# Kernel optimization log

Measured on AMD Instinct MI355X. Metric: run time of the kernel, lower is better.

The kernel has to match this reference:

```python
import jax, jax.numpy as jnp
import numpy as np

NUM_EXPERTS = 4
MLP_RATIO = 4


def setup_inputs() -> dict:
    key = jax.random.key(0)
    k1, k2, k3, k4, k5, k6 = jax.random.split(key, 6)
    B, N, D = 4, 4096, 1024
    OUT = 1024
    H = D * MLP_RATIO
    x = jax.random.normal(k1, (B, N, D), dtype=jnp.float32)
    expert_mask = jax.random.randint(k2, (B, N), 0, NUM_EXPERTS, dtype=jnp.int64)
    w1 = jax.random.normal(k3, (H, D), dtype=jnp.float32) * 0.02
    b1 = jax.random.normal(k4, (H,), dtype=jnp.float32) * 0.02
    w2 = jax.random.normal(k5, (OUT, H), dtype=jnp.float32) * 0.02
    b2 = jax.random.normal(k6, (OUT,), dtype=jnp.float32) * 0.02
    return {"x": x, "expert_mask": expert_mask, "w1": w1, "b1": b1, "w2": w2, "b2": b2}


def reference(x, expert_mask, w1, b1, w2, b2):
    # x: [B, N, D]; expert_mask: [B, N] in [0, NUM_EXPERTS)
    D = x.shape[-1]
    OUT = w2.shape[0]
    E = NUM_EXPERTS
    y = jnp.zeros(x.shape[:-1] + (OUT,), dtype=x.dtype)
    for e in range(E):
        shift = E - 1 - e  # expert E-1 uses full width
        d_in = D >> shift
        d_hid = d_in * MLP_RATIO
        d_out = OUT >> shift
        # nested slice of shared weights
        h = jax.nn.gelu(
            jnp.einsum('bnd,hd->bnh', x[..., :d_in], w1[:d_hid, :d_in]) + b1[:d_hid],
            approximate=False,
        )
        ye = jnp.einsum('bnh,oh->bno', h, w2[:d_out, :d_hid]) + b2[:d_out]
        ye = jnp.pad(ye, ((0, 0), (0, 0), (0, OUT - d_out)))  # zero-fill unused dims
        y = y + jnp.where((expert_mask == e)[..., None], ye, jnp.zeros((), dtype=x.dtype))
    return y
```

## Files before the change

### kernel.cpp

```cpp
#include <hip/hip_runtime.h>
#include <hip/hip_bf16.h>

#define T_TOK 16384
#define DMODEL 1024
#define HDIM 4096
#define OUTD 1024

typedef __attribute__((ext_vector_type(8))) short short8_t;
typedef __attribute__((ext_vector_type(4))) float f32x4;

#define WS_COUNTS_OFF 0
#define WS_LIST_OFF 128
#define WS_XC_OFF   ((size_t)1 << 20)
#define WS_W1BF_OFF ((size_t)34 << 20)
#define WS_W2BF_OFF ((size_t)43 << 20)
#define WS_HBUF_OFF ((size_t)52 << 20)

#define W1N (HDIM * DMODEL)
#define W2N (OUTD * HDIM)

__device__ __forceinline__ short f2bf(float f) {
    union { float f; unsigned u; } x; x.f = f;
    unsigned r = x.u + 0x7FFFu + ((x.u >> 16) & 1u);
    return (short)(r >> 16);
}

__device__ __forceinline__ float gelu_fast(float v) {
    float z = fabsf(v) * 0.7071067811865476f;
    float t = __builtin_amdgcn_rcpf(fmaf(0.3275911f, z, 1.0f));
    float poly = t * fmaf(t, fmaf(t, fmaf(t, fmaf(t, 1.061405429f, -1.453152027f),
                                          1.421413741f), -0.284496736f),
                          0.254829592f);
    float e = fmaf(-poly, __expf(-z * z), 1.0f);
    float erfv = copysignf(e, v);
    return 0.5f * v * (1.0f + erfv);
}

__device__ __forceinline__ void conv8(const float* __restrict__ s, short* __restrict__ d) {
    const float4* s4 = (const float4*)s;
    float4 f0 = s4[0], f1 = s4[1];
    short8_t v;
    v[0] = f2bf(f0.x); v[1] = f2bf(f0.y); v[2] = f2bf(f0.z); v[3] = f2bf(f0.w);
    v[4] = f2bf(f1.x); v[5] = f2bf(f1.y); v[6] = f2bf(f1.z); v[7] = f2bf(f1.w);
    *(short8_t*)d = v;
}

__device__ __forceinline__ void gl_lds16(const short* g, short* lds) {
    __builtin_amdgcn_global_load_lds(
        (const __attribute__((address_space(1))) void*)g,
        (__attribute__((address_space(3))) void*)lds, 16, 0, 0);
}

__device__ __forceinline__ void bases_for(const int* __restrict__ counts, int e,
                                          unsigned long long* hb,
                                          unsigned long long* xb) {
    unsigned long long h = 0, x = 0;
    for (int i = 0; i < e; ++i) {
        unsigned long long c = (unsigned long long)counts[i];
        int din = 128 << i;
        x += c * (unsigned long long)din;
        h += c * (unsigned long long)(din * 4);
    }
    *hb = h; *xb = x;
}

__global__ void k_convert(const float* __restrict__ w1, const float* __restrict__ w2,
                          short* __restrict__ w1bf, short* __restrict__ w2bf,
                          int* counts) {
    if (blockIdx.x == 0 && threadIdx.x < 4) counts[threadIdx.x] = 0;
    size_t elem = ((size_t)blockIdx.x * blockDim.x + threadIdx.x) * 8;
    if (elem < (size_t)W1N) {
        conv8(w1 + elem, w1bf + elem);
    } else {
        size_t o = elem - W1N; conv8(w2 + o, w2bf + o);
    }
}

__global__ void k_build(const int* __restrict__ mask, int* counts, int* list) {
    __shared__ int hcnt[4], hb[4], hpos[4];
    int tid = threadIdx.x;
    if (tid < 4) hcnt[tid] = 0;
    __syncthreads();
    int t = blockIdx.x * 256 + tid;
    int e = mask[t] & 3;
    atomicAdd(&hcnt[e], 1);
    __syncthreads();
    if (tid < 4) { hb[tid] = atomicAdd(&counts[tid], hcnt[tid]); hpos[tid] = 0; }
    __syncthreads();
    int p = atomicAdd(&hpos[e], 1);
    list[e * T_TOK + hb[e] + p] = t;
}

__global__ void k_xgather(const float* __restrict__ x, const int* __restrict__ counts,
                          const int* __restrict__ list, short* __restrict__ xc) {
    const int e = blockIdx.y;
    const int d_in = 128 << e;
    const int cnt = counts[e];
    unsigned long long hbD, xb;
    bases_for(counts, e, &hbD, &xb);
    const size_t nel = (size_t)cnt * d_in;
    const int* lst = list + e * T_TOK;
    short* dst = xc + xb;
    for (size_t idx = ((size_t)blockIdx.x * 256 + threadIdx.x) * 8; idx < nel;
         idx += (size_t)gridDim.x * 256 * 8) {
        int row = (int)(idx >> (7 + e));
        int col = (int)(idx & (d_in - 1));
        int tok = lst[row];
        conv8(x + (size_t)tok * DMODEL + col, dst + idx);
    }
}

__global__ __launch_bounds__(256) void k_pass1(
    const short* __restrict__ xc, const short* __restrict__ w1bf,
    const float* __restrict__ b1, const int* __restrict__ counts,
    short* __restrict__ hbuf)
{
    const int d = blockIdx.x;
    const int xcd = d & 7;
    const int slot = d >> 3;
    const int g = slot >> 6;
    const int bx = slot & 63;
    int e, nt;
    if (g < 4)       { e = 3; nt = xcd * 4 + g; }
    else if (g < 6)  { e = 2; nt = xcd * 2 + (g - 4); }
    else if (g == 6) { e = 1; nt = xcd; }
    else             { if (xcd >= 4) return; e = 0; nt = xcd; }
    const int d_in = 128 << e;
    const int d_hid = d_in * 4;
    const int n0 = nt * 128;
    const int cnt = counts[e];
    unsigned long long hb, xb;
    bases_for(counts, e, &hb, &xb);
    const short* xe = xc + xb;

    __shared__ short Ab[64 * 64];
    __shared__ short Bb[128 * 64];

    const int tid = threadIdx.x;
    const int lane = tid & 63;
    const int w = tid >> 6;
    const int l3 = lane >> 3;
    const int ch = lane & 7;
    const int wm = (w & 1) * 32;
    const int wn = (w >> 1) * 64;

    for (int m0 = bx * 64; m0 < cnt; m0 += 64 * 64) {
        int rA[2];
#pragma unroll
        for (int j = 0; j < 2; ++j) {
            int rr = m0 + j * 32 + w * 8 + l3;
            rA[j] = (rr >= cnt) ? (cnt - 1) : rr;
        }

        f32x4 acc[2][4];
#pragma unroll
        for (int i = 0; i < 2; ++i)
#pragma unroll
            for (int j = 0; j < 4; ++j)
                acc[i][j] = (f32x4){0.f, 0.f, 0.f, 0.f};

        for (int k0 = 0; k0 < d_in; k0 += 64) {
#pragma unroll
            for (int j = 0; j < 2; ++j) {
                int r = j * 32 + w * 8 + l3;
                gl_lds16(xe + (size_t)rA[j] * d_in + k0 + ((ch ^ (r & 7)) << 3),
                         &Ab[(j * 32 + w * 8) * 64]);
            }
#pragma unroll
            for (int j = 0; j < 4; ++j) {
                int r = j * 32 + w * 8 + l3;
                gl_lds16(w1bf + (size_t)(n0 + r) * DMODEL + k0 + ((ch ^ (r & 7)) << 3),
                         &Bb[(j * 32 + w * 8) * 64]);
            }
            __syncthreads();
#pragma unroll
            for (int kk = 0; kk < 2; ++kk) {
                short8_t af[2], bfr[4];
                const int q = (lane >> 4) + kk * 4;
#pragma unroll
                for (int mt = 0; mt < 2; ++mt) {
                    int row = wm + mt * 16 + (lane & 15);
                    af[mt] = *(const short8_t*)&Ab[((row << 3) | (q ^ (row & 7))) << 3];
                }
#pragma unroll
                for (int ntn = 0; ntn < 4; ++ntn) {
                    int row = wn + ntn * 16 + (lane & 15);
                    bfr[ntn] = *(const short8_t*)&Bb[((row << 3) | (q ^ (row & 7))) << 3];
                }
#pragma unroll
                for (int mt = 0; mt < 2; ++mt)
#pragma unroll
                    for (int ntn = 0; ntn < 4; ++ntn)
                        acc[mt][ntn] = __builtin_amdgcn_mfma_f32_16x16x32_bf16(
                            af[mt], bfr[ntn], acc[mt][ntn], 0, 0, 0);
            }
            __syncthreads();
        }

        const int cl = lane & 15;
        const int qr = lane >> 4;
#pragma unroll
        for (int ntn = 0; ntn < 4; ++ntn) {
            int col = n0 + wn + ntn * 16 + cl;
            float bias = b1[col];
#pragma unroll
            for (int mt = 0; mt < 2; ++mt) {
#pragma unroll
                for (int r = 0; r < 4; ++r) {
                    int row = wm + mt * 16 + qr * 4 + r;
                    if (m0 + row < cnt) {
                        float v = acc[mt][ntn][r] + bias;
                        hbuf[hb + (unsigned long long)(m0 + row) * d_hid + col] =
                            f2bf(gelu_fast(v));
                    }
                }
            }
        }
    }
}

__global__ __launch_bounds__(256) void k_pass2(
    const short* __restrict__ hbuf, const short* __restrict__ w2bf,
    const float* __restrict__ b2, const int* __restrict__ counts,
    const int* __restrict__ list, float* __restrict__ y)
{
    const int d = blockIdx.x;
    const int xcd = d & 7;
    const int slot = d >> 3;
    const int g = slot >> 6;
    const int bx = slot & 63;
    if (g == 2) {
        const int z = xcd * 64 + bx;
        const int ch2 = (counts[2] + 63) >> 6, ch1 = (counts[1] + 63) >> 6,
                  ch0 = (counts[0] + 63) >> 6;
        const int n2 = ch2 * 4, n1 = ch1 * 6, n0c = ch0 * 7;
        const int rt = threadIdx.x >> 2;
        const int cq = (threadIdx.x & 3) * 32;
        const float4 z4 = (float4){0.f, 0.f, 0.f, 0.f};
        for (int c = z; c < n2 + n1 + n0c; c += 512) {
            int e, nt, mi, cc = c;
            if (cc < n2)            { e = 2; nt = 4 + cc / ch2; mi = cc % ch2; }
            else { cc -= n2;
                if (cc < n1)        { e = 1; nt = 2 + cc / ch1; mi = cc % ch1; }
                else { cc -= n1;      e = 0; nt = 1 + cc / ch0; mi = cc % ch0; } }
            const int cnt = counts[e];
            int row = mi * 64 + rt;
            if (row < cnt) {
                float* dst = y + (size_t)list[e * T_TOK + row] * OUTD + nt * 128 + cq;
#pragma unroll
                for (int i = 0; i < 8; ++i) *(float4*)(dst + i * 4) = z4;
            }
        }
        return;
    }
    int e, nt;
    if (g == 0) { e = 3; nt = xcd; }
    else {
        if (xcd < 4)       { e = 2; nt = xcd; }
        else if (xcd < 6)  { e = 1; nt = xcd - 4; }
        else if (xcd == 6) { e = 0; nt = 0; }
        else return;
    }
    const int d_in = 128 << e;
    const int d_hid = d_in * 4;
    const int n0 = nt * 128;
    const int cnt = counts[e];
    const int* lst = list + e * T_TOK;
    unsigned long long hb, xb;
    bases_for(counts, e, &hb, &xb);

    __shared__ short Ab[2 * 64 * 64];
    __shared__ short Bb[2 * 128 * 64];

    const int tid = threadIdx.x;
    const int lane = tid & 63;
    const int w = tid >> 6;
    const int l3 = lane >> 3;
    const int ch = lane & 7;
    const int wm = (w & 1) * 32;
    const int wn = (w >> 1) * 64;

#define P2_STAGE(kn, b) do {                                                   \
    _Pragma("unroll") for (int j = 0; j < 2; ++j) {                            \
        int r = j * 32 + w * 8 + l3;                                           \
        gl_lds16(hbuf + hb + (size_t)rA[j] * d_hid + (kn) + ((ch ^ (r & 7)) << 3), \
                 &Ab[(b) * 4096 + (j * 32 + w * 8) * 64]); }                   \
    _Pragma("unroll") for (int j = 0; j < 4; ++j) {                            \
        int r = j * 32 + w * 8 + l3;                                           \
        gl_lds16(w2bf + (size_t)(n0 + r) * HDIM + (kn) + ((ch ^ (r & 7)) << 3), \
                 &Bb[(b) * 8192 + (j * 32 + w * 8) * 64]); }                   \
} while (0)

    for (int m0 = bx * 64; m0 < cnt; m0 += 64 * 64) {
        int rA[2];
#pragma unroll
        for (int j = 0; j < 2; ++j) {
            int rr = m0 + j * 32 + w * 8 + l3;
            rA[j] = (rr >= cnt) ? (cnt - 1) : rr;
        }

        f32x4 acc[2][4];
#pragma unroll
        for (int i = 0; i < 2; ++i)
#pragma unroll
            for (int j = 0; j < 4; ++j)
                acc[i][j] = (f32x4){0.f, 0.f, 0.f, 0.f};

        const int ks = d_hid >> 6;
        P2_STAGE(0, 0);
        for (int kt = 0; kt < ks; ++kt) {
            const int p = kt & 1;
            __builtin_amdgcn_s_barrier();
            if (kt + 1 < ks) {
                P2_STAGE((kt + 1) << 6, 1 - p);
                asm volatile("s_waitcnt vmcnt(6)" ::: "memory");
            } else {
                asm volatile("s_waitcnt vmcnt(0)" ::: "memory");
            }
            __builtin_amdgcn_s_barrier();
            const short* Ap = &Ab[p * 4096];
            const short* Bp = &Bb[p * 8192];
#pragma unroll
            for (int kk = 0; kk < 2; ++kk) {
                short8_t af[2], bfr[4];
                const int q = (lane >> 4) + kk * 4;
#pragma unroll
                for (int mt = 0; mt < 2; ++mt) {
                    int row = wm + mt * 16 + (lane & 15);
                    af[mt] = *(const short8_t*)&Ap[((row << 3) | (q ^ (row & 7))) << 3];
                }
#pragma unroll
                for (int ntn = 0; ntn < 4; ++ntn) {
                    int row = wn + ntn * 16 + (lane & 15);
                    bfr[ntn] = *(const short8_t*)&Bp[((row << 3) | (q ^ (row & 7))) << 3];
                }
#pragma unroll
                for (int mt = 0; mt < 2; ++mt)
#pragma unroll
                    for (int ntn = 0; ntn < 4; ++ntn)
                        acc[mt][ntn] = __builtin_amdgcn_mfma_f32_16x16x32_bf16(
                            af[mt], bfr[ntn], acc[mt][ntn], 0, 0, 0);
            }
        }

        const int cl = lane & 15;
        const int qr = lane >> 4;
#pragma unroll
        for (int ntn = 0; ntn < 4; ++ntn) {
            int col = n0 + wn + ntn * 16 + cl;
            float bias = b2[col];
#pragma unroll
            for (int mt = 0; mt < 2; ++mt) {
#pragma unroll
                for (int r = 0; r < 4; ++r) {
                    int row = wm + mt * 16 + qr * 4 + r;
                    if (m0 + row < cnt) {
                        int tok = lst[m0 + row];
                        y[(size_t)tok * OUTD + col] = acc[mt][ntn][r] + bias;
                    }
                }
            }
        }
    }
#undef P2_STAGE
}

extern "C" void kernel_launch(void* const* d_in, const int* in_sizes, int n_in,
                              void* d_out, int out_size, void* d_ws, size_t ws_size,
                              hipStream_t stream) {
    const float* x  = (const float*)d_in[0];
    const int* mask = (const int*)d_in[1];
    const float* w1 = (const float*)d_in[2];
    const float* b1 = (const float*)d_in[3];
    const float* w2 = (const float*)d_in[4];
    const float* b2 = (const float*)d_in[5];
    float* y = (float*)d_out;

    char* ws = (char*)d_ws;
    int* counts = (int*)(ws + WS_COUNTS_OFF);
    int* list = (int*)(ws + WS_LIST_OFF);
    short* xc   = (short*)(ws + WS_XC_OFF);
    short* w1bf = (short*)(ws + WS_W1BF_OFF);
    short* w2bf = (short*)(ws + WS_W2BF_OFF);
    short* hbuf = (short*)(ws + WS_HBUF_OFF);

    k_convert<<<(W1N + W2N) / 8 / 256, 256, 0, stream>>>(w1, w2, w1bf, w2bf, counts);
    k_build<<<T_TOK / 256, 256, 0, stream>>>(mask, counts, list);
    k_xgather<<<dim3(128, 4), 256, 0, stream>>>(x, counts, list, xc);
    k_pass1<<<4096, 256, 0, stream>>>(xc, w1bf, b1, counts, hbuf);
    k_pass2<<<1536, 256, 0, stream>>>(hbuf, w2bf, b2, counts, list, y);
}
```

Baseline: 359.0 us.

## Split-K expert-3 pass2 across two block groups with atomics; memset output

The g==2 block group no longer zero-fills the unused output columns. It is repurposed as a second K-slice for the full-width expert 3, so expert-3 pass2 work is split across twice as many blocks and combined with float atomicAdd. The output is zeroed up front with hipMemsetAsync, which replaces the per-row zero-fill. The change is meant to rebalance pass2, where expert 3 dominated, at the cost of a full 64MB memset and atomic traffic.

```diff
diff --git a/kernel.cpp b/kernel.cpp
--- a/kernel.cpp
+++ b/kernel.cpp
@@ -229,33 +229,11 @@
     const int slot = d >> 3;
     const int g = slot >> 6;
     const int bx = slot & 63;
-    if (g == 2) {
-        const int z = xcd * 64 + bx;
-        const int ch2 = (counts[2] + 63) >> 6, ch1 = (counts[1] + 63) >> 6,
-                  ch0 = (counts[0] + 63) >> 6;
-        const int n2 = ch2 * 4, n1 = ch1 * 6, n0c = ch0 * 7;
-        const int rt = threadIdx.x >> 2;
-        const int cq = (threadIdx.x & 3) * 32;
-        const float4 z4 = (float4){0.f, 0.f, 0.f, 0.f};
-        for (int c = z; c < n2 + n1 + n0c; c += 512) {
-            int e, nt, mi, cc = c;
-            if (cc < n2)            { e = 2; nt = 4 + cc / ch2; mi = cc % ch2; }
-            else { cc -= n2;
-                if (cc < n1)        { e = 1; nt = 2 + cc / ch1; mi = cc % ch1; }
-                else { cc -= n1;      e = 0; nt = 1 + cc / ch0; mi = cc % ch0; } }
-            const int cnt = counts[e];
-            int row = mi * 64 + rt;
-            if (row < cnt) {
-                float* dst = y + (size_t)list[e * T_TOK + row] * OUTD + nt * 128 + cq;
-#pragma unroll
-                for (int i = 0; i < 8; ++i) *(float4*)(dst + i * 4) = z4;
-            }
-        }
-        return;
-    }
-    int e, nt;
-    if (g == 0) { e = 3; nt = xcd; }
+    int e, nt, kslice;
+    if (g == 0)      { e = 3; nt = xcd; kslice = 0; }
+    else if (g == 1) { e = 3; nt = xcd; kslice = 1; }
     else {
+        kslice = 0;
         if (xcd < 4)       { e = 2; nt = xcd; }
         else if (xcd < 6)  { e = 1; nt = xcd - 4; }
         else if (xcd == 6) { e = 0; nt = 0; }
@@ -268,6 +246,11 @@
     const int* lst = list + e * T_TOK;
     unsigned long long hb, xb;
     bases_for(counts, e, &hb, &xb);
+
+    const int ks_all = d_hid >> 6;
+    const bool split = (e == 3);
+    const int ks0 = split ? kslice * (ks_all >> 1) : 0;
+    const int ks1 = split ? ks0 + (ks_all >> 1) : ks_all;
 
     __shared__ short Ab[2 * 64 * 64];
     __shared__ short Bb[2 * 128 * 64];
@@ -306,12 +289,11 @@
             for (int j = 0; j < 4; ++j)
                 acc[i][j] = (f32x4){0.f, 0.f, 0.f, 0.f};
 
-        const int ks = d_hid >> 6;
-        P2_STAGE(0, 0);
-        for (int kt = 0; kt < ks; ++kt) {
+        P2_STAGE(ks0 << 6, 0);
+        for (int kt = ks0; kt < ks1; ++kt) {
             const int p = kt & 1;
             __builtin_amdgcn_s_barrier();
-            if (kt + 1 < ks) {
+            if (kt + 1 < ks1) {
                 P2_STAGE((kt + 1) << 6, 1 - p);
                 asm volatile("s_waitcnt vmcnt(6)" ::: "memory");
             } else {
@@ -348,7 +330,7 @@
 #pragma unroll
         for (int ntn = 0; ntn < 4; ++ntn) {
             int col = n0 + wn + ntn * 16 + cl;
-            float bias = b2[col];
+            float bias = (kslice == 0) ? b2[col] : 0.f;
 #pragma unroll
             for (int mt = 0; mt < 2; ++mt) {
 #pragma unroll
@@ -356,7 +338,10 @@
                     int row = wm + mt * 16 + qr * 4 + r;
                     if (m0 + row < cnt) {
                         int tok = lst[m0 + row];
-                        y[(size_t)tok * OUTD + col] = acc[mt][ntn][r] + bias;
+                        float v = acc[mt][ntn][r] + bias;
+                        float* dst = &y[(size_t)tok * OUTD + col];
+                        if (split) atomicAdd(dst, v);
+                        else *dst = v;
                     }
                 }
             }
@@ -384,6 +369,8 @@
     short* w2bf = (short*)(ws + WS_W2BF_OFF);
     short* hbuf = (short*)(ws + WS_HBUF_OFF);
 
+    hipMemsetAsync(d_out, 0, (size_t)out_size * sizeof(float), stream);
+
     k_convert<<<(W1N + W2N) / 8 / 256, 256, 0, stream>>>(w1, w2, w1bf, w2bf, counts);
     k_build<<<T_TOK / 256, 256, 0, stream>>>(mask, counts, list);
     k_xgather<<<dim3(128, 4), 256, 0, stream>>>(x, counts, list, xc);
```

Measured after the change: 365.8 us. Within noise of the previous version (+1.9%).
